# Performance work log

Hardware: AMD Instinct MI355X
Metric: run time of the kernel (lower is better)

The kernel has to match this reference:

```python
import jax, jax.numpy as jnp
import numpy as np

K = 8192
D = 512


def setup_inputs() -> dict:
    key = jax.random.key(0)
    k1, k2 = jax.random.split(key)
    x = jax.random.normal(k1, (64, 512, 512), dtype=jnp.float32)
    # nn.Embedding(K, D) with weight.uniform_(-1/K, 1/K)
    codebook = jax.random.uniform(k2, (K, D), dtype=jnp.float32,
                                  minval=-1.0 / K, maxval=1.0 / K)
    return {"x": x, "codebook": codebook}


def reference(x, codebook):
    # vq(x, codebook): nearest-neighbor codebook indices.
    d = codebook.shape[1]
    flat = x.reshape(-1, d)                              # [N, D]
    cb_sqr = jnp.sum(codebook * codebook, axis=1)        # [K]
    dists = cb_sqr[None, :] - 2.0 * jnp.einsum('nd,kd->nk', flat, codebook)  # [N, K]
    indices = jnp.argmin(dists, axis=1).astype(jnp.int32)
    return indices.reshape(x.shape[:-1])                 # latents = indices
```

## Files before the change

kernel.cpp:

```cpp
#include <hip/hip_runtime.h>


#define D_DIM 512
#define EPS_GAP 0.082f
#define KSPLIT 8

typedef __attribute__((ext_vector_type(16))) float f32x16;
typedef _Float16 half8v __attribute__((ext_vector_type(8)));
typedef _Float16 half4v __attribute__((ext_vector_type(4)));

__device__ __forceinline__ void gload_lds16(const void* g, void* l) {
    __builtin_amdgcn_global_load_lds(
        (const __attribute__((address_space(1))) unsigned int*)g,
        (__attribute__((address_space(3))) unsigned int*)l, 16, 0, 0);
}

__device__ __forceinline__ void ins3(float d, int i, float& d1, int& i1,
                                     float& d2, int& i2, float& d3) {
    if (d < d1 || (d == d1 && i < i1)) { d3 = d2; d2 = d1; i2 = i1; d1 = d; i1 = i; }
    else if (d < d2 || (d == d2 && i < i2)) { d3 = d2; d2 = d; i2 = i; }
    else if (d < d3) d3 = d;
}

__global__ __launch_bounds__(256) void prep_kernel(
        const float* __restrict__ X, const float* __restrict__ CB,
        _Float16* __restrict__ XT, _Float16* __restrict__ Ch,
        float* __restrict__ cbs, int* __restrict__ cnt,
        int K, int cbBlocks) {
    const int bid = blockIdx.x;
    const int tid = threadIdx.x;
    if (bid == 0 && tid == 0) *cnt = 0;
    if (bid < cbBlocks) {
        int w = bid * 4 + (tid >> 6);
        int lane = tid & 63;
        if (w >= K) return;
        size_t base = (size_t)w * D_DIM + lane * 8;
        const float4* r4 = (const float4*)(CB + base);
        float4 u = r4[0], v = r4[1];
        float s = u.x*u.x + u.y*u.y + u.z*u.z + u.w*u.w
                + v.x*v.x + v.y*v.y + v.z*v.z + v.w*v.w;
        half8v h;
        h[0] = (_Float16)(u.x * 4096.f); h[1] = (_Float16)(u.y * 4096.f);
        h[2] = (_Float16)(u.z * 4096.f); h[3] = (_Float16)(u.w * 4096.f);
        h[4] = (_Float16)(v.x * 4096.f); h[5] = (_Float16)(v.y * 4096.f);
        h[6] = (_Float16)(v.z * 4096.f); h[7] = (_Float16)(v.w * 4096.f);
        *(half8v*)(Ch + base) = h;
#pragma unroll
        for (int off = 32; off; off >>= 1) s += __shfl_xor(s, off);
        if (lane == 0) cbs[w] = s;
    } else {
        const int tile = bid - cbBlocks;
        const int o  = tid & 63;
        const int rq = tid >> 6;
        half8v* XT8 = (half8v*)XT;
#pragma unroll 4
        for (int rr = 0; rr < 16; ++rr) {
            int r = rq * 16 + rr;
            size_t src = (size_t)(tile * 64 + r) * D_DIM + o * 8;
            float4 a = *(const float4*)&X[src];
            float4 b = *(const float4*)&X[src + 4];
            half8v h;
            h[0] = (_Float16)a.x; h[1] = (_Float16)a.y;
            h[2] = (_Float16)a.z; h[3] = (_Float16)a.w;
            h[4] = (_Float16)b.x; h[5] = (_Float16)b.y;
            h[6] = (_Float16)b.z; h[7] = (_Float16)b.w;
            XT8[tile * 4096 + o * 64 + r] = h;
        }
    }
}

__global__ __launch_bounds__(512, 2) void vq_mfma_kernel(
        const _Float16* __restrict__ XT, const _Float16* __restrict__ Ch,
        const float* __restrict__ cbs,
        float* __restrict__ pd1, int* __restrict__ pi1,
        float* __restrict__ pd2, int* __restrict__ pi2,
        float* __restrict__ pd3, int N, int K) {

    __shared__ _Float16 Cs[3][256 * 32];

    const int tid  = threadIdx.x;
    const int lane = tid & 63;
    const int w    = tid >> 6;
    const int wr   = w >> 2;
    const int wcq  = w & 3;
    const int bid  = blockIdx.x;
    const int split     = bid & (KSPLIT - 1);
    const int rowBase   = (bid >> 3) * 256;
    const int kPerSplit = K / KSPLIT;
    const int splitBase = split * kPerSplit;
    const int NT        = kPerSplit / 256;
    const int nSteps    = NT * 16;

    const int l4  = lane >> 2;
    const int swz = ((lane & 3) ^ ((lane >> 3) & 3)) * 8;
    const int sflip = (swz ^ 16) - swz;
    const size_t gC0 = (size_t)(w * 32 + l4) * D_DIM + swz;
    const int l0 = w * 1024 + lane * 8;

    const int lh = lane >> 5;
    const int rC = wr * 128 + (lane & 31);
    const int kp = ((lane >> 1) & 3) ^ (((lane >> 4) & 1) << 1);
    const int kOff0 = (lh ^ kp) * 8;
    const int kOff1 = kOff0 ^ 16;

    const half8v* XT8 = (const half8v*)XT;
    const int xb0 = ((rowBase >> 6) + wcq) * 4096 + lh * 64 + (lane & 31);

    float d1v[2], d2v[2], d3v[2];
    int   i1v[2], i2v[2];
#pragma unroll
    for (int nf = 0; nf < 2; ++nf) {
        d1v[nf] = 3.4e38f; d2v[nf] = 3.4e38f; d3v[nf] = 3.4e38f;
        i1v[nf] = 0x7fffffff; i2v[nf] = 0x7fffffff;
    }

    f32x16 acc[4][2];

    auto fold = [&](int ctF) {
        const int cb0 = splitBase + ctF * 256 + wr * 128 + 4 * lh;
#pragma unroll
        for (int mf = 0; mf < 4; ++mf)
#pragma unroll
            for (int rq = 0; rq < 4; ++rq) {
                float4 c2q = *(const float4*)&cbs[cb0 + mf * 32 + rq * 8];
#pragma unroll
                for (int j = 0; j < 4; ++j) {
                    const int code = cb0 + mf * 32 + rq * 8 + j;
                    const int reg  = rq * 4 + j;
                    const float c2 = (&c2q.x)[j] * 4096.f;
#pragma unroll
                    for (int nf = 0; nf < 2; ++nf) {
                        float dist = fmaf(-2.f, acc[mf][nf][reg], c2);
                        ins3(dist, code, d1v[nf], i1v[nf], d2v[nf], i2v[nf], d3v[nf]);
                    }
                }
            }
    };

#define STAGE(buf, s_)                                                        \
    do { int ct_ = (s_) >> 4, kt_ = (s_) & 15;                                \
        size_t cb_ = (size_t)(splitBase + ct_ * 256) * D_DIM + gC0 + kt_ * 32;\
        gload_lds16(Ch + cb_,                        &Cs[buf][l0]);           \
        gload_lds16(Ch + cb_ + 16 * D_DIM + sflip,   &Cs[buf][l0 + 512]);     \
    } while (0)

    STAGE(0, 0);
    STAGE(1, 1);
    half8v xvC[2][2], xvN[2][2];
#pragma unroll
    for (int nf = 0; nf < 2; ++nf)
#pragma unroll
        for (int kh = 0; kh < 2; ++kh)
            xvC[nf][kh] = XT8[xb0 + kh * 128 + nf * 32];

    int bufR = 0, bufW = 2;

    for (int s = 0; s < nSteps; ++s) {
        const int kt = s & 15;
        const int ct = s >> 4;

        if (s + 2 < nSteps) {
            asm volatile("s_waitcnt vmcnt(6)" ::: "memory");
        } else {
            asm volatile("s_waitcnt vmcnt(0)" ::: "memory");
        }
        __builtin_amdgcn_s_barrier();
        __builtin_amdgcn_sched_barrier(0);

        if (s + 2 < nSteps) STAGE(bufW, s + 2);
        if (s + 1 < nSteps) {
            const int kt1 = (s + 1) & 15;
#pragma unroll
            for (int nf = 0; nf < 2; ++nf)
#pragma unroll
                for (int kh = 0; kh < 2; ++kh)
                    xvN[nf][kh] = XT8[xb0 + kt1 * 256 + kh * 128 + nf * 32];
        }

        half8v cv[4][2];
#pragma unroll
        for (int mf = 0; mf < 4; ++mf) {
            cv[mf][0] = *(const half8v*)&Cs[bufR][(rC + mf * 32) * 32 + kOff0];
            cv[mf][1] = *(const half8v*)&Cs[bufR][(rC + mf * 32) * 32 + kOff1];
        }

        if (kt == 0) {
            if (s) fold(ct - 1);
#pragma unroll
            for (int mf = 0; mf < 4; ++mf)
#pragma unroll
                for (int nf = 0; nf < 2; ++nf)
#pragma unroll
                    for (int r = 0; r < 16; ++r) acc[mf][nf][r] = 0.f;
        }

#pragma unroll
        for (int kh = 0; kh < 2; ++kh)
#pragma unroll
            for (int mf = 0; mf < 4; ++mf)
#pragma unroll
                for (int nf = 0; nf < 2; ++nf)
                    acc[mf][nf] = __builtin_amdgcn_mfma_f32_32x32x16_f16(
                        cv[mf][kh], xvC[nf][kh], acc[mf][nf], 0, 0, 0);

#pragma unroll
        for (int nf = 0; nf < 2; ++nf)
#pragma unroll
            for (int kh = 0; kh < 2; ++kh)
                xvC[nf][kh] = xvN[nf][kh];

        if (++bufR == 3) bufR = 0;
        if (++bufW == 3) bufW = 0;
    }
#undef STAGE

    fold(NT - 1);

#pragma unroll
    for (int nf = 0; nf < 2; ++nf) {
        float od1 = __shfl_xor(d1v[nf], 32);
        int   oi1 = __shfl_xor(i1v[nf], 32);
        float od2 = __shfl_xor(d2v[nf], 32);
        int   oi2 = __shfl_xor(i2v[nf], 32);
        float od3 = __shfl_xor(d3v[nf], 32);
        ins3(od1, oi1, d1v[nf], i1v[nf], d2v[nf], i2v[nf], d3v[nf]);
        ins3(od2, oi2, d1v[nf], i1v[nf], d2v[nf], i2v[nf], d3v[nf]);
        d3v[nf] = fminf(d3v[nf], od3);
    }

    __syncthreads();
    float* mD1 = (float*)&Cs[0][0];
    int*   mI1 = (int*)(mD1 + 256);
    float* mD2 = (float*)(mD1 + 512);
    int*   mI2 = (int*)(mD1 + 768);
    float* mD3 = (float*)(mD1 + 1024);
    if (wr == 1 && lane < 32) {
#pragma unroll
        for (int nf = 0; nf < 2; ++nf) {
            int x = wcq * 64 + nf * 32 + (lane & 31);
            mD1[x] = d1v[nf]; mI1[x] = i1v[nf];
            mD2[x] = d2v[nf]; mI2[x] = i2v[nf];
            mD3[x] = d3v[nf];
        }
    }
    __syncthreads();
    if (wr == 0 && lane < 32) {
#pragma unroll
        for (int nf = 0; nf < 2; ++nf) {
            int x = wcq * 64 + nf * 32 + (lane & 31);
            float d1 = d1v[nf], d2 = d2v[nf], d3 = d3v[nf];
            int i1 = i1v[nf], i2 = i2v[nf];
            ins3(mD1[x], mI1[x], d1, i1, d2, i2, d3);
            ins3(mD2[x], mI2[x], d1, i1, d2, i2, d3);
            d3 = fminf(d3, mD3[x]);
            size_t p = (size_t)split * N + (rowBase + x);
            pd1[p] = d1; pi1[p] = i1; pd2[p] = d2; pi2[p] = i2; pd3[p] = d3;
        }
    }
}

__global__ __launch_bounds__(256) void combine_kernel(
        const float* __restrict__ X, const float* __restrict__ CB,
        const float* __restrict__ cbs,
        const float* __restrict__ pd1, const int* __restrict__ pi1,
        const float* __restrict__ pd2, const int* __restrict__ pi2,
        const float* __restrict__ pd3,
        int* __restrict__ out, int* __restrict__ flags, int* __restrict__ cnt,
        int N, int S) {
    const int row = blockIdx.x * 256 + threadIdx.x;
    if (row >= N) return;
    float d1 = pd1[row], d2 = pd2[row], d3 = pd3[row];
    int i1 = pi1[row], i2 = pi2[row];
    for (int s = 1; s < S; ++s) {
        size_t p = (size_t)s * N + row;
        ins3(pd1[p], pi1[p], d1, i1, d2, i2, d3);
        ins3(pd2[p], pi2[p], d1, i1, d2, i2, d3);
        d3 = fminf(d3, pd3[p]);
    }
    int best = i1;
    if (d2 - d1 < EPS_GAP) {
        if (d3 - d1 < EPS_GAP) {
            int f = atomicAdd(cnt, 1);
            flags[f] = row;
        } else {
            const float4* xr = (const float4*)(X + (size_t)row * D_DIM);
            const float4* ca = (const float4*)(CB + (size_t)i1 * D_DIM);
            const float4* cb = (const float4*)(CB + (size_t)i2 * D_DIM);
            float dotA = 0.f, dotB = 0.f;
#pragma unroll 4
            for (int d = 0; d < D_DIM / 4; ++d) {
                float4 xv = xr[d], av = ca[d], bv = cb[d];
                dotA = fmaf(xv.x, av.x, dotA); dotA = fmaf(xv.y, av.y, dotA);
                dotA = fmaf(xv.z, av.z, dotA); dotA = fmaf(xv.w, av.w, dotA);
                dotB = fmaf(xv.x, bv.x, dotB); dotB = fmaf(xv.y, bv.y, dotB);
                dotB = fmaf(xv.z, bv.z, dotB); dotB = fmaf(xv.w, bv.w, dotB);
            }
            float dA = fmaf(-2.f, dotA, cbs[i1]);
            float dB = fmaf(-2.f, dotB, cbs[i2]);
            best = (dB < dA || (dB == dA && i2 < i1)) ? i2 : i1;
        }
    }
    out[row] = best;
}

__global__ __launch_bounds__(256) void rare_scan_kernel(
        const float* __restrict__ X, const float* __restrict__ CB,
        const float* __restrict__ cbs,
        const int* __restrict__ flags, const int* __restrict__ cnt,
        float* __restrict__ scrD, int* __restrict__ scrI, int K) {
    __shared__ float xs[D_DIM];
    __shared__ float rD[4];
    __shared__ int   rI[4];
    const int nTasks = (*cnt) * 32;
    const int cpc = K / 32;
    for (int t = blockIdx.x; t < nTasks; t += gridDim.x) {
        const int fi = t >> 5, chunk = t & 31;
        const int row = flags[fi];
        __syncthreads();
        for (int i = threadIdx.x; i < D_DIM; i += 256)
            xs[i] = X[(size_t)row * D_DIM + i];
        __syncthreads();
        float bd = 3.4e38f; int bi = 0x7fffffff;
        for (int c = chunk * cpc + threadIdx.x; c < (chunk + 1) * cpc; c += 256) {
            const float4* cp = (const float4*)(CB + (size_t)c * D_DIM);
            float dot = 0.f;
#pragma unroll 4
            for (int d = 0; d < D_DIM / 4; ++d) {
                float4 cv = cp[d];
                float4 xv = *(const float4*)&xs[d * 4];
                dot = fmaf(xv.x, cv.x, dot); dot = fmaf(xv.y, cv.y, dot);
                dot = fmaf(xv.z, cv.z, dot); dot = fmaf(xv.w, cv.w, dot);
            }
            float dist = fmaf(-2.f, dot, cbs[c]);
            if (dist < bd || (dist == bd && c < bi)) { bd = dist; bi = c; }
        }
#pragma unroll
        for (int off = 1; off < 64; off <<= 1) {
            float od = __shfl_xor(bd, off);
            int   oi = __shfl_xor(bi, off);
            if (od < bd || (od == bd && oi < bi)) { bd = od; bi = oi; }
        }
        if ((threadIdx.x & 63) == 0) { rD[threadIdx.x >> 6] = bd; rI[threadIdx.x >> 6] = bi; }
        __syncthreads();
        if (threadIdx.x == 0) {
            for (int ww = 1; ww < 4; ++ww)
                if (rD[ww] < bd || (rD[ww] == bd && rI[ww] < bi)) {
                    bd = rD[ww]; bi = rI[ww];
                }
            scrD[t] = bd; scrI[t] = bi;
        }
    }
}

__global__ __launch_bounds__(256) void rare_write_kernel(
        const int* __restrict__ flags, const int* __restrict__ cnt,
        const float* __restrict__ scrD, const int* __restrict__ scrI,
        int* __restrict__ out) {
    const int nf = *cnt;
    for (int fi = blockIdx.x * 256 + threadIdx.x; fi < nf;
         fi += gridDim.x * 256) {
        float bd = scrD[fi * 32]; int bi = scrI[fi * 32];
        for (int ch = 1; ch < 32; ++ch) {
            float d = scrD[fi * 32 + ch]; int i = scrI[fi * 32 + ch];
            if (d < bd || (d == bd && i < bi)) { bd = d; bi = i; }
        }
        out[flags[fi]] = bi;
    }
}

#define BM 128
#define BN 128
#define BD 16

__global__ __launch_bounds__(256) void cbsqr_kernel(const float* __restrict__ cb,
                                                    float* __restrict__ out, int K) {
    int gtid = blockIdx.x * blockDim.x + threadIdx.x;
    int w = gtid >> 6;
    int lane = gtid & 63;
    if (w >= K) return;
    const float4* r4 = (const float4*)(cb + (size_t)w * D_DIM) + lane * 2;
    float4 u = r4[0], v = r4[1];
    float s = u.x*u.x + u.y*u.y + u.z*u.z + u.w*u.w
            + v.x*v.x + v.y*v.y + v.z*v.z + v.w*v.w;
#pragma unroll
    for (int off = 32; off; off >>= 1) s += __shfl_xor(s, off);
    if (lane == 0) out[w] = s;
}

__global__ __launch_bounds__(128) void vq_fp32_kernel(
        const float* __restrict__ X, const float* __restrict__ CB,
        const float* __restrict__ cbs,
        float* __restrict__ pd, int* __restrict__ pi,
        int* __restrict__ out, int N, int K, int nsplit) {

    __shared__ float As[BD][BM + 4];
    __shared__ float Bs[BD][BN + 4];

    const int tid = threadIdx.x;
    const int tx = tid & 7;
    const int ty = tid >> 3;
    const int rowBase = blockIdx.x * BM;
    const int split = blockIdx.y;
    const int kPer = K / nsplit;
    const int c0 = split * kPer, c1 = c0 + kPer;
    const int ldRow = tid >> 2;
    const int ldCol = (tid & 3) * 4;

    float bestD[8]; int bestI[8];
#pragma unroll
    for (int i = 0; i < 8; ++i) { bestD[i] = 3.4e38f; bestI[i] = 0; }

    for (int ct = c0; ct < c1; ct += BN) {
        float acc[8][16];
#pragma unroll
        for (int i = 0; i < 8; ++i)
#pragma unroll
            for (int j = 0; j < 16; ++j) acc[i][j] = 0.f;

        for (int dt = 0; dt < D_DIM; dt += BD) {
#pragma unroll
            for (int p = 0; p < 4; ++p) {
                int r = ldRow + p * 32;
                float4 av = *(const float4*)&X[(size_t)(rowBase + r) * D_DIM + dt + ldCol];
                float4 bv = *(const float4*)&CB[(size_t)(ct + r) * D_DIM + dt + ldCol];
                As[ldCol + 0][r] = av.x; As[ldCol + 1][r] = av.y;
                As[ldCol + 2][r] = av.z; As[ldCol + 3][r] = av.w;
                Bs[ldCol + 0][r] = bv.x; Bs[ldCol + 1][r] = bv.y;
                Bs[ldCol + 2][r] = bv.z; Bs[ldCol + 3][r] = bv.w;
            }
            __syncthreads();
#pragma unroll
            for (int d = 0; d < BD; ++d) {
                float4 a0 = *(const float4*)&As[d][ty * 4];
                float4 a1 = *(const float4*)&As[d][64 + ty * 4];
                float4 b0 = *(const float4*)&Bs[d][ 0 + tx * 4];
                float4 b1 = *(const float4*)&Bs[d][32 + tx * 4];
                float4 b2 = *(const float4*)&Bs[d][64 + tx * 4];
                float4 b3 = *(const float4*)&Bs[d][96 + tx * 4];
                float a[8] = {a0.x,a0.y,a0.z,a0.w,a1.x,a1.y,a1.z,a1.w};
                float b[16] = {b0.x,b0.y,b0.z,b0.w, b1.x,b1.y,b1.z,b1.w,
                               b2.x,b2.y,b2.z,b2.w, b3.x,b3.y,b3.z,b3.w};
#pragma unroll
                for (int i = 0; i < 8; ++i)
#pragma unroll
                    for (int j = 0; j < 16; ++j)
                        acc[i][j] = fmaf(a[i], b[j], acc[i][j]);
            }
            __syncthreads();
        }
#pragma unroll
        for (int j = 0; j < 16; ++j) {
            int code = ct + (j >> 2) * 32 + tx * 4 + (j & 3);
            float c2v = cbs[code];
#pragma unroll
            for (int i = 0; i < 8; ++i) {
                float dist = fmaf(-2.f, acc[i][j], c2v);
                if (dist < bestD[i]) { bestD[i] = dist; bestI[i] = code; }
            }
        }
    }
#pragma unroll
    for (int i = 0; i < 8; ++i) {
        float bd = bestD[i]; int bi = bestI[i];
#pragma unroll
        for (int off = 1; off < 8; off <<= 1) {
            float od = __shfl_xor(bd, off);
            int   oi = __shfl_xor(bi, off);
            if (od < bd || (od == bd && oi < bi)) { bd = od; bi = oi; }
        }
        if (tx == 0) {
            int row = rowBase + ((i < 4) ? ty * 4 + i : 64 + ty * 4 + (i - 4));
            if (nsplit == 1) out[row] = bi;
            else {
                pd[(size_t)row * nsplit + split] = bd;
                pi[(size_t)row * nsplit + split] = bi;
            }
        }
    }
}

__global__ __launch_bounds__(256) void combine_fp32_kernel(
        const float* __restrict__ pd, const int* __restrict__ pi,
        int* __restrict__ out, int N, int S) {
    int r = blockIdx.x * blockDim.x + threadIdx.x;
    if (r >= N) return;
    float bd = pd[(size_t)r * S];
    int bi = pi[(size_t)r * S];
    for (int s = 1; s < S; ++s) {
        float d = pd[(size_t)r * S + s];
        int i = pi[(size_t)r * S + s];
        if (d < bd || (d == bd && i < bi)) { bd = d; bi = i; }
    }
    out[r] = bi;
}

extern "C" void kernel_launch(void* const* d_in, const int* in_sizes, int n_in,
                              void* d_out, int out_size, void* d_ws, size_t ws_size,
                              hipStream_t stream) {
    const float* X  = (const float*)d_in[0];
    const float* CB = (const float*)d_in[1];
    const int N = in_sizes[0] / D_DIM;
    const int K = in_sizes[1] / D_DIM;
    int* out = (int*)d_out;

    size_t o = 0;
    auto take = [&](size_t bytes) { size_t r = o; o += (bytes + 255) & ~(size_t)255; return r; };
    size_t oCbs = take((size_t)K * 4);
    size_t oXT  = take((size_t)N * D_DIM * 2);
    size_t oCh  = take((size_t)K * D_DIM * 2);
    size_t oPd1 = take((size_t)N * KSPLIT * 4);
    size_t oPi1 = take((size_t)N * KSPLIT * 4);
    size_t oPd2 = take((size_t)N * KSPLIT * 4);
    size_t oPi2 = take((size_t)N * KSPLIT * 4);
    size_t oPd3 = take((size_t)N * KSPLIT * 4);
    size_t oFlg = take((size_t)N * 4);
    size_t oCnt = take(256);
    size_t oScD = take((size_t)N * 32 * 4);
    size_t oScI = take((size_t)N * 32 * 4);
    const size_t need = o;

    char* ws = (char*)d_ws;
    float* cbs = (float*)(ws + oCbs);

    if (ws_size >= need && (N % 256) == 0 && (K % (KSPLIT * 256)) == 0 &&
        (K % 32) == 0) {
        _Float16* XT = (_Float16*)(ws + oXT);
        _Float16* Ch = (_Float16*)(ws + oCh);
        float* pd1 = (float*)(ws + oPd1);
        int*   pi1 = (int*)(ws + oPi1);
        float* pd2 = (float*)(ws + oPd2);
        int*   pi2 = (int*)(ws + oPi2);
        float* pd3 = (float*)(ws + oPd3);
        int* flags = (int*)(ws + oFlg);
        int* cnt   = (int*)(ws + oCnt);
        float* scrD = (float*)(ws + oScD);
        int*   scrI = (int*)(ws + oScI);

        const int cbBlocks = K / 4;
        const int xTiles   = N / 64;
        prep_kernel<<<cbBlocks + xTiles, 256, 0, stream>>>(
            X, CB, XT, Ch, cbs, cnt, K, cbBlocks);

        vq_mfma_kernel<<<(N / 256) * KSPLIT, 512, 0, stream>>>(
            XT, Ch, cbs, pd1, pi1, pd2, pi2, pd3, N, K);

        combine_kernel<<<N / 256, 256, 0, stream>>>(
            X, CB, cbs, pd1, pi1, pd2, pi2, pd3, out, flags, cnt, N, KSPLIT);

        rare_scan_kernel<<<1024, 256, 0, stream>>>(
            X, CB, cbs, flags, cnt, scrD, scrI, K);

        rare_write_kernel<<<32, 256, 0, stream>>>(flags, cnt, scrD, scrI, out);
    } else {
        size_t base = ((size_t)K * 4 + 255) & ~(size_t)255;
        int nsplit = 4;
        while (nsplit > 1 &&
               (ws_size < base + (size_t)N * nsplit * 8 || (K % (nsplit * BN)) != 0))
            nsplit >>= 1;
        float* pd = (float*)(ws + base);
        int*   pi = (int*)(ws + base + (size_t)N * nsplit * 4);
        cbsqr_kernel<<<(K + 3) / 4, 256, 0, stream>>>(CB, cbs, K);
        dim3 grid(N / BM, nsplit);
        vq_fp32_kernel<<<grid, 128, 0, stream>>>(X, CB, cbs, pd, pi, out, N, K, nsplit);
        if (nsplit > 1)
            combine_fp32_kernel<<<(N + 255) / 256, 256, 0, stream>>>(pd, pi, out, N, nsplit);
    }
}
```

Measured before the change: 666.5 us.

## Stream codebook fragments directly from a pre-tiled global layout into registers

The prep kernel now writes the fp16 codebook in the same tiled fragment layout already used for X. The MFMA kernel then loads codebook operands straight from global memory into registers with one-step prefetch, instead of staging through a triple-buffered LDS pipeline with barriers. The codebook squared norms are cached in LDS once per block. This removes LDS traffic and per-step barriers, but each wave now loads codebook tiles separately, so global and L2 traffic rises and there is less latency hiding.

```diff
diff --git a/kernel.cpp b/kernel.cpp
--- a/kernel.cpp
+++ b/kernel.cpp
@@ -7,13 +7,6 @@
 
 typedef __attribute__((ext_vector_type(16))) float f32x16;
 typedef _Float16 half8v __attribute__((ext_vector_type(8)));
-typedef _Float16 half4v __attribute__((ext_vector_type(4)));
-
-__device__ __forceinline__ void gload_lds16(const void* g, void* l) {
-    __builtin_amdgcn_global_load_lds(
-        (const __attribute__((address_space(1))) unsigned int*)g,
-        (__attribute__((address_space(3))) unsigned int*)l, 16, 0, 0);
-}
 
 __device__ __forceinline__ void ins3(float d, int i, float& d1, int& i1,
                                      float& d2, int& i2, float& d3) {
@@ -24,7 +17,7 @@
 
 __global__ __launch_bounds__(256) void prep_kernel(
         const float* __restrict__ X, const float* __restrict__ CB,
-        _Float16* __restrict__ XT, _Float16* __restrict__ Ch,
+        _Float16* __restrict__ XT, _Float16* __restrict__ CT,
         float* __restrict__ cbs, int* __restrict__ cnt,
         int K, int cbBlocks) {
     const int bid = blockIdx.x;
@@ -44,7 +37,7 @@
         h[2] = (_Float16)(u.z * 4096.f); h[3] = (_Float16)(u.w * 4096.f);
         h[4] = (_Float16)(v.x * 4096.f); h[5] = (_Float16)(v.y * 4096.f);
         h[6] = (_Float16)(v.z * 4096.f); h[7] = (_Float16)(v.w * 4096.f);
-        *(half8v*)(Ch + base) = h;
+        ((half8v*)CT)[(w >> 6) * 4096 + lane * 64 + (w & 63)] = h;
 #pragma unroll
         for (int off = 32; off; off >>= 1) s += __shfl_xor(s, off);
         if (lane == 0) cbs[w] = s;
@@ -70,13 +63,14 @@
 }
 
 __global__ __launch_bounds__(512, 2) void vq_mfma_kernel(
-        const _Float16* __restrict__ XT, const _Float16* __restrict__ Ch,
+        const _Float16* __restrict__ XT, const _Float16* __restrict__ CT,
         const float* __restrict__ cbs,
         float* __restrict__ pd1, int* __restrict__ pi1,
         float* __restrict__ pd2, int* __restrict__ pi2,
         float* __restrict__ pd3, int N, int K) {
 
-    __shared__ _Float16 Cs[3][256 * 32];
+    __shared__ float cbsS[1024];
+    __shared__ float mrg[1280];
 
     const int tid  = threadIdx.x;
     const int lane = tid & 63;
@@ -91,20 +85,15 @@
     const int NT        = kPerSplit / 256;
     const int nSteps    = NT * 16;
 
-    const int l4  = lane >> 2;
-    const int swz = ((lane & 3) ^ ((lane >> 3) & 3)) * 8;
-    const int sflip = (swz ^ 16) - swz;
-    const size_t gC0 = (size_t)(w * 32 + l4) * D_DIM + swz;
-    const int l0 = w * 1024 + lane * 8;
-
-    const int lh = lane >> 5;
-    const int rC = wr * 128 + (lane & 31);
-    const int kp = ((lane >> 1) & 3) ^ (((lane >> 4) & 1) << 1);
-    const int kOff0 = (lh ^ kp) * 8;
-    const int kOff1 = kOff0 ^ 16;
+    for (int i = tid; i < kPerSplit; i += 512) cbsS[i] = cbs[splitBase + i];
+    __syncthreads();
 
     const half8v* XT8 = (const half8v*)XT;
-    const int xb0 = ((rowBase >> 6) + wcq) * 4096 + lh * 64 + (lane & 31);
+    const half8v* CT8 = (const half8v*)CT;
+    const int lhl = lane & 31;
+    const int lh  = lane >> 5;
+    const int cb00 = ((splitBase >> 6) + wr * 2) * 4096 + lh * 64 + lhl;
+    const int xb0  = ((rowBase >> 6) + wcq) * 4096 + lh * 64 + lhl;
 
     float d1v[2], d2v[2], d3v[2];
     int   i1v[2], i2v[2];
@@ -117,15 +106,15 @@
     f32x16 acc[4][2];
 
     auto fold = [&](int ctF) {
-        const int cb0 = splitBase + ctF * 256 + wr * 128 + 4 * lh;
+        const int cl0 = ctF * 256 + wr * 128 + 4 * lh;
 #pragma unroll
         for (int mf = 0; mf < 4; ++mf)
 #pragma unroll
             for (int rq = 0; rq < 4; ++rq) {
-                float4 c2q = *(const float4*)&cbs[cb0 + mf * 32 + rq * 8];
+                float4 c2q = *(const float4*)&cbsS[cl0 + mf * 32 + rq * 8];
 #pragma unroll
                 for (int j = 0; j < 4; ++j) {
-                    const int code = cb0 + mf * 32 + rq * 8 + j;
+                    const int code = splitBase + cl0 + mf * 32 + rq * 8 + j;
                     const int reg  = rq * 4 + j;
                     const float c2 = (&c2q.x)[j] * 4096.f;
 #pragma unroll
@@ -137,51 +126,38 @@
             }
     };
 
-#define STAGE(buf, s_)                                                        \
-    do { int ct_ = (s_) >> 4, kt_ = (s_) & 15;                                \
-        size_t cb_ = (size_t)(splitBase + ct_ * 256) * D_DIM + gC0 + kt_ * 32;\
-        gload_lds16(Ch + cb_,                        &Cs[buf][l0]);           \
-        gload_lds16(Ch + cb_ + 16 * D_DIM + sflip,   &Cs[buf][l0 + 512]);     \
-    } while (0)
-
-    STAGE(0, 0);
-    STAGE(1, 1);
-    half8v xvC[2][2], xvN[2][2];
+    half8v cvC[4][2], cvN[4][2], xvC[2][2], xvN[2][2];
+
+#pragma unroll
+    for (int mf = 0; mf < 4; ++mf)
+#pragma unroll
+        for (int kh = 0; kh < 2; ++kh)
+            cvC[mf][kh] = CT8[cb00 + (mf >> 1) * 4096 + (kh * 2) * 64 + (mf & 1) * 32];
 #pragma unroll
     for (int nf = 0; nf < 2; ++nf)
 #pragma unroll
         for (int kh = 0; kh < 2; ++kh)
-            xvC[nf][kh] = XT8[xb0 + kh * 128 + nf * 32];
-
-    int bufR = 0, bufW = 2;
+            xvC[nf][kh] = XT8[xb0 + (kh * 2) * 64 + nf * 32];
 
     for (int s = 0; s < nSteps; ++s) {
         const int kt = s & 15;
         const int ct = s >> 4;
 
-        if (s + 2 < nSteps) {
-            asm volatile("s_waitcnt vmcnt(6)" ::: "memory");
-        } else {
-            asm volatile("s_waitcnt vmcnt(0)" ::: "memory");
-        }
-        __builtin_amdgcn_s_barrier();
-        __builtin_amdgcn_sched_barrier(0);
-
-        if (s + 2 < nSteps) STAGE(bufW, s + 2);
         if (s + 1 < nSteps) {
             const int kt1 = (s + 1) & 15;
+            const int ct1 = (s + 1) >> 4;
+            const int cb1 = cb00 + ct1 * 4 * 4096 + kt1 * 4 * 64;
+            const int xb1 = xb0 + kt1 * 4 * 64;
+#pragma unroll
+            for (int mf = 0; mf < 4; ++mf)
+#pragma unroll
+                for (int kh = 0; kh < 2; ++kh)
+                    cvN[mf][kh] = CT8[cb1 + (mf >> 1) * 4096 + kh * 128 + (mf & 1) * 32];
 #pragma unroll
             for (int nf = 0; nf < 2; ++nf)
 #pragma unroll
                 for (int kh = 0; kh < 2; ++kh)
-                    xvN[nf][kh] = XT8[xb0 + kt1 * 256 + kh * 128 + nf * 32];
-        }
-
-        half8v cv[4][2];
-#pragma unroll
-        for (int mf = 0; mf < 4; ++mf) {
-            cv[mf][0] = *(const half8v*)&Cs[bufR][(rC + mf * 32) * 32 + kOff0];
-            cv[mf][1] = *(const half8v*)&Cs[bufR][(rC + mf * 32) * 32 + kOff1];
+                    xvN[nf][kh] = XT8[xb1 + kh * 128 + nf * 32];
         }
 
         if (kt == 0) {
@@ -201,18 +177,19 @@
 #pragma unroll
                 for (int nf = 0; nf < 2; ++nf)
                     acc[mf][nf] = __builtin_amdgcn_mfma_f32_32x32x16_f16(
-                        cv[mf][kh], xvC[nf][kh], acc[mf][nf], 0, 0, 0);
-
+                        cvC[mf][kh], xvC[nf][kh], acc[mf][nf], 0, 0, 0);
+
+#pragma unroll
+        for (int mf = 0; mf < 4; ++mf)
+#pragma unroll
+            for (int kh = 0; kh < 2; ++kh)
+                cvC[mf][kh] = cvN[mf][kh];
 #pragma unroll
         for (int nf = 0; nf < 2; ++nf)
 #pragma unroll
             for (int kh = 0; kh < 2; ++kh)
                 xvC[nf][kh] = xvN[nf][kh];
-
-        if (++bufR == 3) bufR = 0;
-        if (++bufW == 3) bufW = 0;
-    }
-#undef STAGE
+    }
 
     fold(NT - 1);
 
@@ -229,15 +206,15 @@
     }
 
     __syncthreads();
-    float* mD1 = (float*)&Cs[0][0];
-    int*   mI1 = (int*)(mD1 + 256);
-    float* mD2 = (float*)(mD1 + 512);
-    int*   mI2 = (int*)(mD1 + 768);
-    float* mD3 = (float*)(mD1 + 1024);
+    float* mD1 = mrg;
+    int*   mI1 = (int*)(mrg + 256);
+    float* mD2 = mrg + 512;
+    int*   mI2 = (int*)(mrg + 768);
+    float* mD3 = mrg + 1024;
     if (wr == 1 && lane < 32) {
 #pragma unroll
         for (int nf = 0; nf < 2; ++nf) {
-            int x = wcq * 64 + nf * 32 + (lane & 31);
+            int x = wcq * 64 + nf * 32 + lhl;
             mD1[x] = d1v[nf]; mI1[x] = i1v[nf];
             mD2[x] = d2v[nf]; mI2[x] = i2v[nf];
             mD3[x] = d3v[nf];
@@ -247,7 +224,7 @@
     if (wr == 0 && lane < 32) {
 #pragma unroll
         for (int nf = 0; nf < 2; ++nf) {
-            int x = wcq * 64 + nf * 32 + (lane & 31);
+            int x = wcq * 64 + nf * 32 + lhl;
             float d1 = d1v[nf], d2 = d2v[nf], d3 = d3v[nf];
             int i1 = i1v[nf], i2 = i2v[nf];
             ins3(mD1[x], mI1[x], d1, i1, d2, i2, d3);
@@ -507,7 +484,7 @@
     auto take = [&](size_t bytes) { size_t r = o; o += (bytes + 255) & ~(size_t)255; return r; };
     size_t oCbs = take((size_t)K * 4);
     size_t oXT  = take((size_t)N * D_DIM * 2);
-    size_t oCh  = take((size_t)K * D_DIM * 2);
+    size_t oCT  = take((size_t)K * D_DIM * 2);
     size_t oPd1 = take((size_t)N * KSPLIT * 4);
     size_t oPi1 = take((size_t)N * KSPLIT * 4);
     size_t oPd2 = take((size_t)N * KSPLIT * 4);
@@ -525,7 +502,7 @@
     if (ws_size >= need && (N % 256) == 0 && (K % (KSPLIT * 256)) == 0 &&
         (K % 32) == 0) {
         _Float16* XT = (_Float16*)(ws + oXT);
-        _Float16* Ch = (_Float16*)(ws + oCh);
+        _Float16* CT = (_Float16*)(ws + oCT);
         float* pd1 = (float*)(ws + oPd1);
         int*   pi1 = (int*)(ws + oPi1);
         float* pd2 = (float*)(ws + oPd2);
@@ -539,10 +516,10 @@
         const int cbBlocks = K / 4;
         const int xTiles   = N / 64;
         prep_kernel<<<cbBlocks + xTiles, 256, 0, stream>>>(
-            X, CB, XT, Ch, cbs, cnt, K, cbBlocks);
+            X, CB, XT, CT, cbs, cnt, K, cbBlocks);
 
         vq_mfma_kernel<<<(N / 256) * KSPLIT, 512, 0, stream>>>(
-            XT, Ch, cbs, pd1, pi1, pd2, pi2, pd3, N, K);
+            XT, CT, cbs, pd1, pi1, pd2, pi2, pd3, N, K);
 
         combine_kernel<<<N / 256, 256, 0, stream>>>(
             X, CB, cbs, pd1, pi1, pd2, pi2, pd3, out, flags, cnt, N, KSPLIT);
```

New measurement: 600.8 us. 1.11x faster.
